# Kernel optimization log

Hardware: AMD Instinct MI355X
Metric: run time of the kernel (lower is better)

## Reference

```python
import jax, jax.numpy as jnp
import numpy as np
import math

B, L, D, H, DFF = 2, 2048, 1024, 16, 4096

def _mha(xq, xkv, Wq, bq, Wk, bk, Wv, bv, Wo, bo, mask, h):
    # xq: [B,Lq,D], xkv: [B,Lk,D], mask: [B,1,Lq,Lk] bool
    b, lq, d = xq.shape
    dk = d // h
    q = (xq @ Wq + bq).reshape(b, lq, h, dk).transpose(0, 2, 1, 3)        # [B,h,Lq,dk]
    k = (xkv @ Wk + bk).reshape(b, -1, h, dk).transpose(0, 2, 1, 3)       # [B,h,Lk,dk]
    v = (xkv @ Wv + bv).reshape(b, -1, h, dk).transpose(0, 2, 1, 3)       # [B,h,Lk,dk]
    scores = jnp.einsum('bhqd,bhkd->bhqk', q, k) / jnp.sqrt(jnp.float32(dk))
    scores = jnp.where(mask, scores, jnp.float32(-1e9))                   # masked_fill(mask==0, -1e9)
    prob = jax.nn.softmax(scores, axis=-1)
    out = jnp.einsum('bhqk,bhkd->bhqd', prob, v)
    out = out.transpose(0, 2, 1, 3).reshape(b, lq, d)
    return out @ Wo + bo

def setup_inputs() -> dict:
    key = jax.random.key(0)
    ks = jax.random.split(key, 16)
    s = 0.02
    inp = {
        'tgt': jax.random.normal(ks[0], (B, L, D), jnp.float32),
        'encoder_out': jax.random.normal(ks[1], (B, L, D), jnp.float32),
        'tgt_mask': jnp.broadcast_to(jnp.tril(jnp.ones((L, L), bool)), (B, 1, L, L)),
        'src_tgt_mask': jnp.ones((B, 1, L, L), bool),
    }
    names = ['sWq','sWk','sWv','sWo','cWq','cWk','cWv','cWo']
    for i, n in enumerate(names):
        inp[n] = s * jax.random.normal(ks[2 + i], (D, D), jnp.float32)
        inp['sb' + n[2] if n[0] == 's' else 'cb' + n[2]] = jnp.zeros((D,), jnp.float32)
    inp['W1'] = s * jax.random.normal(ks[10], (D, DFF), jnp.float32)
    inp['b1'] = jnp.zeros((DFF,), jnp.float32)
    inp['W2'] = s * jax.random.normal(ks[11], (DFF, D), jnp.float32)
    inp['b2'] = jnp.zeros((D,), jnp.float32)
    return inp

def reference(tgt, encoder_out, tgt_mask, src_tgt_mask,
              sWq, sbq, sWk, sbk, sWv, sbv, sWo, sbo,
              cWq, cbq, cWk, cbk, cWv, cbv, cWo, cbo,
              W1, b1, W2, b2):
    # residual 1: masked self-attention (no norm)
    x = tgt + _mha(tgt, tgt, sWq, sbq, sWk, sbk, sWv, sbv, sWo, sbo, tgt_mask, H)
    # residual 2: cross-attention over encoder_out
    x = x + _mha(x, encoder_out, cWq, cbq, cWk, cbk, cWv, cbv, cWo, cbo, src_tgt_mask, H)
    # residual 3: position-wise FFN with ReLU
    x = x + (jax.nn.relu(x @ W1 + b1) @ W2 + b2)
    return x
```

## Files before the change

kernel.cpp:

```cpp
#include <hip/hip_runtime.h>

typedef unsigned short u16;
typedef unsigned int u32;
typedef __attribute__((ext_vector_type(8))) short short8;
typedef __attribute__((ext_vector_type(8))) __bf16 bf16x8;
typedef __attribute__((ext_vector_type(4))) float f32x4;
typedef __attribute__((ext_vector_type(4))) u16 u16x4;
typedef __attribute__((ext_vector_type(2))) u32 u32x2;

#define GLD16(gp, lp) __builtin_amdgcn_global_load_lds( \
    (const __attribute__((address_space(1))) unsigned int*)(gp), \
    (__attribute__((address_space(3))) unsigned int*)(lp), 16, 0, 0)

#if defined(__has_builtin) && __has_builtin(__builtin_amdgcn_exp2f)
#define EXP2(x) __builtin_amdgcn_exp2f(x)
#else
static __device__ __forceinline__ float exp2_asm(float x){
  float r; asm("v_exp_f32 %0, %1" : "=v"(r) : "v"(x)); return r;
}
#define EXP2(x) exp2_asm(x)
#endif

__device__ __forceinline__ float bf2f(u16 u){
  unsigned x = ((unsigned)u) << 16; float f; __builtin_memcpy(&f, &x, 4); return f;
}
__device__ __forceinline__ u16 f2bf(float f){
  unsigned x; __builtin_memcpy(&x, &f, 4);
  x += 0x7fffu + ((x >> 16) & 1u);
  return (u16)(x >> 16);
}
__device__ __forceinline__ u32 pkhi(float lo, float hi){
  u32 a, b; __builtin_memcpy(&a, &lo, 4); __builtin_memcpy(&b, &hi, 4);
  return __builtin_amdgcn_perm(b, a, 0x07060302u);
}
__device__ __forceinline__ f32x4 mfma_bf16(short8 a, short8 b, f32x4 c){
  return __builtin_amdgcn_mfma_f32_16x16x32_bf16(
      __builtin_bit_cast(bf16x8, a), __builtin_bit_cast(bf16x8, b), c, 0, 0, 0);
}

__global__ __launch_bounds__(256) void k_conv(const float* __restrict__ s, u16* __restrict__ d, int n){
  int i4 = (blockIdx.x * 256 + threadIdx.x) * 4;
  if (i4 < n){
    float4 v = *(const float4*)(s + i4);
    u16x4 o; o.x = f2bf(v.x); o.y = f2bf(v.y); o.z = f2bf(v.z); o.w = f2bf(v.w);
    *(u16x4*)(d + i4) = o;
  }
}

__global__ __launch_bounds__(256) void k_transpose(const float* __restrict__ s, u16* __restrict__ d, int K, int N){
  __shared__ float t[32][33];
  int bx = blockIdx.x * 32, by = blockIdx.y * 32;
  int x = threadIdx.x & 31, y = threadIdx.x >> 5;
  #pragma unroll
  for (int i = 0; i < 4; i++)
    t[y + i*8][x] = s[(size_t)(by + y + i*8) * N + bx + x];
  __syncthreads();
  #pragma unroll
  for (int i = 0; i < 4; i++)
    d[(size_t)(bx + y + i*8) * K + by + x] = f2bf(t[x][y + i*8]);
}

struct TP8 { const float* s[8]; u16* d[8]; };
__global__ __launch_bounds__(256) void k_transpose8(TP8 p){
  __shared__ float t[32][33];
  const float* s = p.s[blockIdx.z];
  u16* d = p.d[blockIdx.z];
  int bx = blockIdx.x * 32, by = blockIdx.y * 32;
  int x = threadIdx.x & 31, y = threadIdx.x >> 5;
  #pragma unroll
  for (int i = 0; i < 4; i++)
    t[y + i*8][x] = s[(size_t)(by + y + i*8) * 1024 + bx + x];
  __syncthreads();
  #pragma unroll
  for (int i = 0; i < 4; i++)
    d[(size_t)(bx + y + i*8) * 1024 + by + x] = f2bf(t[x][y + i*8]);
}

__global__ __launch_bounds__(256) void k_packbias(
    const float* __restrict__ sbq, const float* __restrict__ sbk,
    const float* __restrict__ sbv, const float* __restrict__ cbk,
    const float* __restrict__ cbv, float* __restrict__ pbS,
    float* __restrict__ pbC){
  int i = blockIdx.x * 256 + threadIdx.x;
  if (i < 3072) pbS[i] = (i < 1024) ? sbq[i] : (i < 2048 ? sbk[i-1024] : sbv[i-2048]);
  if (i < 2048) pbC[i] = (i < 1024) ? cbk[i] : cbv[i-1024];
}

template<int EPI, int BM, int BN, int KU>
__global__ __launch_bounds__(256, 2) void k_gemm_bt(
    const u16* __restrict__ A, const u16* __restrict__ BT,
    const float* __restrict__ bias, const float* __restrict__ resid,
    float* __restrict__ outF, u16* __restrict__ outB,
    int M, int N, int K, int vt_start, u16* __restrict__ Vt){
  constexpr int MI = BM / 32, NI = BN / 32;
  __shared__ u16 As[2*KU][BM*32];
  __shared__ u16 Bs[2*KU][BN*32];
  int tid = threadIdx.x, wave = tid >> 6, lane = tid & 63;
  int bm = blockIdx.x * BM, bn = blockIdx.y * BN;
  int wm = (wave & 1) * (BM/2), wn = (wave >> 1) * (BN/2);
  int l15 = lane & 15, quad = lane >> 4;

  f32x4 z = {0.f, 0.f, 0.f, 0.f};
  f32x4 acc[MI][NI];
  #pragma unroll
  for (int a = 0; a < MI; a++)
    #pragma unroll
    for (int b = 0; b < NI; b++) acc[a][b] = z;

  int sr = wave*16 + (lane >> 2);
  int sc = ((lane & 3) ^ ((lane >> 3) & 3)) * 8;
  const u16* Ag = A  + (size_t)(bm + sr) * K + sc;
  const u16* Bg = BT + (size_t)(bn + sr) * K + sc;
  int NKP = (K >> 5) / KU;
  int xsw = (l15 >> 1) & 3;

  #pragma unroll
  for (int u = 0; u < KU; u++){
    #pragma unroll
    for (int i = 0; i < BM/64; i++)
      GLD16(Ag + (size_t)(i*64)*K + u*32, &As[u][(wave*16 + i*64) * 32]);
    #pragma unroll
    for (int i = 0; i < BN/64; i++)
      GLD16(Bg + (size_t)(i*64)*K + u*32, &Bs[u][(wave*16 + i*64) * 32]);
  }

  for (int kt = 0; kt < NKP; kt++){
    __syncthreads();
    int cur = (kt & 1) * KU;
    if (kt + 1 < NKP){
      int nb = cur ^ KU;
      #pragma unroll
      for (int u = 0; u < KU; u++){
        int k0 = ((kt + 1) * KU + u) * 32;
        #pragma unroll
        for (int i = 0; i < BM/64; i++)
          GLD16(Ag + (size_t)(i*64)*K + k0, &As[nb+u][(wave*16 + i*64) * 32]);
        #pragma unroll
        for (int i = 0; i < BN/64; i++)
          GLD16(Bg + (size_t)(i*64)*K + k0, &Bs[nb+u][(wave*16 + i*64) * 32]);
      }
    }
    #pragma unroll
    for (int u = 0; u < KU; u++){
      short8 af[MI], bf[NI];
      #pragma unroll
      for (int mi = 0; mi < MI; mi++)
        af[mi] = *(const short8*)&As[cur+u][(wm + mi*16 + l15)*32 + (quad ^ xsw)*8];
      #pragma unroll
      for (int ni = 0; ni < NI; ni++)
        bf[ni] = *(const short8*)&Bs[cur+u][(wn + ni*16 + l15)*32 + (quad ^ xsw)*8];
      #pragma unroll
      for (int mi = 0; mi < MI; mi++)
        #pragma unroll
        for (int ni = 0; ni < NI; ni++)
          acc[mi][ni] = mfma_bf16(af[mi], bf[ni], acc[mi][ni]);
    }
  }

  #pragma unroll
  for (int mi = 0; mi < MI; mi++){
    #pragma unroll
    for (int ni = 0; ni < NI; ni++){
      int col = bn + wn + ni*16 + l15;
      float bv = bias[col];
      if (EPI == 0 && col >= vt_start){
        int vc = col - vt_start;
        int hh = vc >> 6, dd = vc & 63;
        int row0 = bm + wm + mi*16 + quad*4;
        int bb = row0 >> 11, ll = row0 & 2047;
        u16x4 vv;
        #pragma unroll
        for (int r = 0; r < 4; r++) vv[r] = f2bf(acc[mi][ni][r] + bv);
        *(u16x4*)&Vt[(((size_t)bb*16 + hh)*64 + dd)*2048 + ll] = vv;
      } else {
        #pragma unroll
        for (int r = 0; r < 4; r++){
          int row = bm + wm + mi*16 + quad*4 + r;
          float v = acc[mi][ni][r] + bv;
          if (EPI == 1) v = v > 0.f ? v : 0.f;
          size_t idx = (size_t)row * N + col;
          if (EPI >= 2) v += resid[idx];
          if (EPI == 2 || EPI == 3) outF[idx] = v;
          if (EPI != 3) outB[idx] = f2bf(v);
        }
      }
    }
  }
}

template<int EPI>
__global__ __launch_bounds__(256, 4) void k_gemm64(
    const u16* __restrict__ A, const u16* __restrict__ BT,
    const float* __restrict__ bias, const float* __restrict__ resid,
    float* __restrict__ outF, u16* __restrict__ outB,
    int M, int N, int K){
  __shared__ u16 As[4][64*32];
  __shared__ u16 Bs[4][64*32];
  int tid = threadIdx.x, wave = tid >> 6, lane = tid & 63;
  int bm = blockIdx.x * 64, bn = blockIdx.y * 64;
  int wm = (wave & 1) * 32, wn = (wave >> 1) * 32;
  int l15 = lane & 15, quad = lane >> 4;

  f32x4 z = {0.f, 0.f, 0.f, 0.f};
  f32x4 acc[2][2];
  acc[0][0] = z; acc[0][1] = z; acc[1][0] = z; acc[1][1] = z;

  int sr = wave*16 + (lane >> 2);
  int sc = ((lane & 3) ^ ((lane >> 3) & 3)) * 8;
  const u16* Ag = A  + (size_t)(bm + sr) * K + sc;
  const u16* Bg = BT + (size_t)(bn + sr) * K + sc;
  int NT = K >> 5;
  int xsw = (l15 >> 1) & 3;

  #pragma unroll
  for (int s = 0; s < 3; s++){
    GLD16(Ag + s*32, &As[s][(wave*16) * 32]);
    GLD16(Bg + s*32, &Bs[s][(wave*16) * 32]);
  }

  for (int kt = 0; kt < NT; kt++){
    if (kt < NT-2)       asm volatile("s_waitcnt vmcnt(4)" ::: "memory");
    else if (kt == NT-2) asm volatile("s_waitcnt vmcnt(2)" ::: "memory");
    else                 asm volatile("s_waitcnt vmcnt(0)" ::: "memory");
    __builtin_amdgcn_s_barrier();
    if (kt + 3 < NT){
      int s = (kt + 3) & 3, k0 = (kt + 3) * 32;
      GLD16(Ag + k0, &As[s][(wave*16) * 32]);
      GLD16(Bg + k0, &Bs[s][(wave*16) * 32]);
    }
    int cur = kt & 3;
    short8 af[2], bf[2];
    af[0] = *(const short8*)&As[cur][(wm      + l15)*32 + (quad ^ xsw)*8];
    af[1] = *(const short8*)&As[cur][(wm + 16 + l15)*32 + (quad ^ xsw)*8];
    bf[0] = *(const short8*)&Bs[cur][(wn      + l15)*32 + (quad ^ xsw)*8];
    bf[1] = *(const short8*)&Bs[cur][(wn + 16 + l15)*32 + (quad ^ xsw)*8];
    acc[0][0] = mfma_bf16(af[0], bf[0], acc[0][0]);
    acc[0][1] = mfma_bf16(af[0], bf[1], acc[0][1]);
    acc[1][0] = mfma_bf16(af[1], bf[0], acc[1][0]);
    acc[1][1] = mfma_bf16(af[1], bf[1], acc[1][1]);
  }

  #pragma unroll
  for (int mi = 0; mi < 2; mi++){
    #pragma unroll
    for (int ni = 0; ni < 2; ni++){
      int col = bn + wn + ni*16 + l15;
      float bv = bias[col];
      #pragma unroll
      for (int r = 0; r < 4; r++){
        int row = bm + wm + mi*16 + quad*4 + r;
        float v = acc[mi][ni][r] + bv;
        size_t idx = (size_t)row * N + col;
        if (EPI >= 2) v += resid[idx];
        if (EPI == 2 || EPI == 3) outF[idx] = v;
        if (EPI != 3) outB[idx] = f2bf(v);
      }
    }
  }
}

template<bool CAUSAL>
__global__ __launch_bounds__(256, 2) void k_flash(
    const u16* __restrict__ Q, int ldq,
    const u16* __restrict__ Kg, int ldk,
    const u16* __restrict__ Vt,
    u16* __restrict__ O, int ldo){
  __shared__ u16 Ks[2][128*64];
  __shared__ u16 Vs[2][64*128];
  __shared__ u16 Ps[128*64];
  int tid = threadIdx.x, wave = tid >> 6, lane = tid & 63;
  int l15 = lane & 15, quad = lane >> 4;
  int bx = blockIdx.x;
  int qt = CAUSAL ? ((bx & 1) ? (15 - (bx >> 1)) : (bx >> 1)) : bx;
  int bh = blockIdx.y;
  int b = bh >> 4, h = bh & 15;
  size_t bL = (size_t)b * 2048;
  const u16* qp = Q  + (bL + qt*128) * (size_t)ldq + h*64;
  const u16* kp = Kg + bL * (size_t)ldk + h*64;
  const u16* vtp = Vt + (size_t)bh * 64 * 2048;
  int wm = wave * 32;

  const float QSCALE = 0.125f * 1.44269504088896f;
  short8 qf[2][2];
  #pragma unroll
  for (int mi = 0; mi < 2; mi++)
    #pragma unroll
    for (int ks = 0; ks < 2; ks++){
      short8 t = *(const short8*)(qp + (size_t)(wm + mi*16 + l15)*ldq + ks*32 + quad*8);
      #pragma unroll
      for (int j = 0; j < 8; j++)
        t[j] = (short)f2bf(bf2f((u16)t[j]) * QSCALE);
      qf[mi][ks] = t;
    }

  f32x4 z = {0.f, 0.f, 0.f, 0.f};
  f32x4 o[2][4];
  float mrow[2], lrow[2];
  #pragma unroll
  for (int mi = 0; mi < 2; mi++){ mrow[mi] = -3.0e38f; lrow[mi] = 0.f; }
  #pragma unroll
  for (int mi = 0; mi < 2; mi++)
    #pragma unroll
    for (int nd = 0; nd < 4; nd++) o[mi][nd] = z;

  int nkt = CAUSAL ? (qt + 1) : 16;
  int cg = ((lane & 7) ^ ((lane >> 3) & 7)) * 8;
  #pragma unroll
  for (int i = 0; i < 4; i++){
    int r = i*32 + wave*8 + (lane >> 3);
    GLD16(kp + (size_t)r * ldk + cg, &Ks[0][(i*32 + wave*8) * 64]);
  }
  #pragma unroll
  for (int i = 0; i < 4; i++){
    int d0 = i*16 + wave*4;
    int d = d0 + (lane >> 4);
    int j = lane & 15;
    int chunk = (j & 8) | ((j ^ (d & 7)) & 7);
    GLD16(vtp + (size_t)d*2048 + chunk*8, &Vs[0][d0*128]);
  }

  for (int kt = 0; kt < nkt; kt++){
    __syncthreads();
    int cur = kt & 1;
    if (kt + 1 < nkt){
      int nb = cur ^ 1;
      #pragma unroll
      for (int i = 0; i < 4; i++){
        int r = i*32 + wave*8 + (lane >> 3);
        GLD16(kp + (size_t)((kt+1)*128 + r) * ldk + cg, &Ks[nb][(i*32 + wave*8) * 64]);
      }
      #pragma unroll
      for (int i = 0; i < 4; i++){
        int d0 = i*16 + wave*4;
        int d = d0 + (lane >> 4);
        int j = lane & 15;
        int chunk = (j & 8) | ((j ^ (d & 7)) & 7);
        GLD16(vtp + (size_t)d*2048 + (kt+1)*128 + chunk*8, &Vs[nb][d0*128]);
      }
    }

    f32x4 s[2][8];
    #pragma unroll
    for (int mi = 0; mi < 2; mi++)
      #pragma unroll
      for (int nk = 0; nk < 8; nk++) s[mi][nk] = z;
    #pragma unroll
    for (int ks = 0; ks < 2; ks++){
      short8 kf[8];
      #pragma unroll
      for (int nk = 0; nk < 8; nk++){
        int row = nk*16 + l15;
        kf[nk] = *(const short8*)&Ks[cur][row*64 + (((ks*4 + quad) ^ (row & 7)))*8];
      }
      #pragma unroll
      for (int mi = 0; mi < 2; mi++)
        #pragma unroll
        for (int nk = 0; nk < 8; nk++)
          s[mi][nk] = mfma_bf16(kf[nk], qf[mi][ks], s[mi][nk]);
    }

    if (CAUSAL && kt == qt){
      #pragma unroll
      for (int mi = 0; mi < 2; mi++){
        int q = wm + mi*16 + l15;
        #pragma unroll
        for (int nk = 0; nk < 8; nk++)
          #pragma unroll
          for (int r = 0; r < 4; r++){
            int key = nk*16 + quad*4 + r;
            if (key > q) s[mi][nk][r] = -1e30f;
          }
      }
    }

    #pragma unroll
    for (int mi = 0; mi < 2; mi++){
      float mx = s[mi][0][0];
      #pragma unroll
      for (int nk = 0; nk < 8; nk++)
        #pragma unroll
        for (int r = 0; r < 4; r++) mx = fmaxf(mx, s[mi][nk][r]);
      mx = fmaxf(mx, __shfl_xor(mx, 16));
      mx = fmaxf(mx, __shfl_xor(mx, 32));
      if (!__all(mx - mrow[mi] <= 8.f)){
        float mnew = fmaxf(mrow[mi], mx);
        float alpha = EXP2(mrow[mi] - mnew);
        mrow[mi] = mnew;
        lrow[mi] *= alpha;
        #pragma unroll
        for (int r = 0; r < 4; r++){
          float ar = __shfl(alpha, quad*20 + r);
          #pragma unroll
          for (int nd = 0; nd < 4; nd++) o[mi][nd][r] *= ar;
        }
      }
      float ls = 0.f;
      #pragma unroll
      for (int nk = 0; nk < 8; nk++)
        #pragma unroll
        for (int r = 0; r < 4; r++){
          float p = EXP2(s[mi][nk][r] - mrow[mi]);
          s[mi][nk][r] = p;
          ls += p;
        }
      ls += __shfl_xor(ls, 16);
      ls += __shfl_xor(ls, 32);
      lrow[mi] += ls;
    }

    #pragma unroll
    for (int half = 0; half < 2; half++){
      #pragma unroll
      for (int mi = 0; mi < 2; mi++){
        int row = wm + mi*16 + l15;
        #pragma unroll
        for (int nkl = 0; nkl < 4; nkl++){
          int nk = half*4 + nkl;
          u32x2 pw;
          pw.x = pkhi(s[mi][nk][0], s[mi][nk][1]);
          pw.y = pkhi(s[mi][nk][2], s[mi][nk][3]);
          int c = nkl*4 + quad;
          int phys = c ^ (row & 14);
          *(u32x2*)&Ps[row*64 + phys*4] = pw;
        }
      }
      #pragma unroll
      for (int kcl = 0; kcl < 2; kcl++){
        int kc = half*2 + kcl;
        short8 vf[4], pf[2];
        #pragma unroll
        for (int nd = 0; nd < 4; nd++){
          int d = nd*16 + l15;
          int cc = kc*4 + quad;
          int phys = (cc & 8) | ((cc ^ (d & 7)) & 7);
          vf[nd] = *(const short8*)&Vs[cur][d*128 + phys*8];
        }
        #pragma unroll
        for (int mi = 0; mi < 2; mi++){
          int row = wm + mi*16 + l15;
          int pc = kcl*8 + quad*2;
          int pphys = pc ^ (row & 14);
          pf[mi] = *(const short8*)&Ps[row*64 + pphys*4];
        }
        #pragma unroll
        for (int mi = 0; mi < 2; mi++)
          #pragma unroll
          for (int nd = 0; nd < 4; nd++)
            o[mi][nd] = mfma_bf16(pf[mi], vf[nd], o[mi][nd]);
      }
    }
  }

  u16* op = O + (bL + qt*128) * (size_t)ldo + h*64;
  #pragma unroll
  for (int mi = 0; mi < 2; mi++){
    float invl = 1.f / lrow[mi];
    #pragma unroll
    for (int r = 0; r < 4; r++){
      float ir = __shfl(invl, quad*20 + r);
      #pragma unroll
      for (int nd = 0; nd < 4; nd++)
        op[(size_t)(wm + mi*16 + quad*4 + r)*ldo + nd*16 + l15] = f2bf(o[mi][nd][r] * ir);
    }
  }
}

extern "C" void kernel_launch(void* const* d_in, const int* in_sizes, int n_in,
                              void* d_out, int out_size, void* d_ws, size_t ws_size,
                              hipStream_t stream){
  (void)in_sizes; (void)n_in; (void)out_size; (void)ws_size;
  const float* tgt = (const float*)d_in[0];
  const float* enc = (const float*)d_in[1];
  const float* sWq = (const float*)d_in[4];  const float* sbq = (const float*)d_in[5];
  const float* sWk = (const float*)d_in[6];  const float* sbk = (const float*)d_in[7];
  const float* sWv = (const float*)d_in[8];  const float* sbv = (const float*)d_in[9];
  const float* sWo = (const float*)d_in[10]; const float* sbo = (const float*)d_in[11];
  const float* cWq = (const float*)d_in[12]; const float* cbq = (const float*)d_in[13];
  const float* cWk = (const float*)d_in[14]; const float* cbk = (const float*)d_in[15];
  const float* cWv = (const float*)d_in[16]; const float* cbv = (const float*)d_in[17];
  const float* cWo = (const float*)d_in[18]; const float* cbo = (const float*)d_in[19];
  const float* W1  = (const float*)d_in[20]; const float* b1  = (const float*)d_in[21];
  const float* W2  = (const float*)d_in[22]; const float* b2  = (const float*)d_in[23];
  float* out = (float*)d_out;

  const int M = 4096;
  const int NEVER = 1 << 30;
  char* w = (char*)d_ws;
  auto alloc = [&](size_t bytes)->void*{ void* p = w; w += (bytes + 255) & ~(size_t)255; return p; };
  u16* tb    = (u16*)alloc((size_t)M*1024*2);
  u16* eb    = (u16*)alloc((size_t)M*1024*2);
  u16* qkv   = (u16*)alloc((size_t)M*3072*2);
  u16* ao    = (u16*)alloc((size_t)M*1024*2);
  u16* xb    = (u16*)alloc((size_t)M*1024*2);
  float* x1f = (float*)alloc((size_t)M*1024*4);
  u16* hbuf  = (u16*)alloc((size_t)M*4096*2);
  u16* VtS   = (u16*)alloc((size_t)32*64*2048*2);
  u16* VtC   = (u16*)alloc((size_t)32*64*2048*2);
  u16* sQKVT = (u16*)alloc((size_t)3072*1024*2);
  u16* sWoT  = (u16*)alloc((size_t)1024*1024*2);
  u16* cWqT  = (u16*)alloc((size_t)1024*1024*2);
  u16* cKVT  = (u16*)alloc((size_t)2048*1024*2);
  u16* cWoT  = (u16*)alloc((size_t)1024*1024*2);
  u16* W1T   = (u16*)alloc((size_t)4096*1024*2);
  u16* W2T   = (u16*)alloc((size_t)1024*4096*2);
  float* pbS = (float*)alloc(3072*4);
  float* pbC = (float*)alloc(2048*4);
  u16* cq  = tb;
  u16* ckv = qkv;

  k_conv<<<dim3(4096), 256, 0, stream>>>(tgt, tb, M*1024);
  k_conv<<<dim3(4096), 256, 0, stream>>>(enc, eb, M*1024);
  TP8 tp;
  tp.s[0]=sWq; tp.s[1]=sWk; tp.s[2]=sWv; tp.s[3]=sWo;
  tp.s[4]=cWq; tp.s[5]=cWk; tp.s[6]=cWv; tp.s[7]=cWo;
  tp.d[0]=sQKVT; tp.d[1]=sQKVT+1024*1024; tp.d[2]=sQKVT+2048*1024; tp.d[3]=sWoT;
  tp.d[4]=cWqT; tp.d[5]=cKVT; tp.d[6]=cKVT+1024*1024; tp.d[7]=cWoT;
  k_transpose8<<<dim3(32,32,8), 256, 0, stream>>>(tp);
  k_transpose<<<dim3(128,32), 256, 0, stream>>>(W1, W1T, 1024, 4096);
  k_transpose<<<dim3(32,128), 256, 0, stream>>>(W2, W2T, 4096, 1024);
  k_packbias<<<dim3(12), 256, 0, stream>>>(sbq, sbk, sbv, cbk, cbv, pbS, pbC);

  k_gemm_bt<0,128,128,1><<<dim3(32,24), 256, 0, stream>>>(tb, sQKVT, pbS, nullptr, nullptr, qkv, M, 3072, 1024, 2048, VtS);
  k_flash<true><<<dim3(16,32), 256, 0, stream>>>(qkv, 3072, qkv+1024, 3072, VtS, ao, 1024);
  k_gemm64<2><<<dim3(64,16), 256, 0, stream>>>(ao, sWoT, sbo, tgt, x1f, xb, M, 1024, 1024);

  k_gemm64<0><<<dim3(64,16), 256, 0, stream>>>(xb, cWqT, cbq, nullptr, nullptr, cq, M, 1024, 1024);
  k_gemm_bt<0,128,128,1><<<dim3(32,16), 256, 0, stream>>>(eb, cKVT, pbC, nullptr, nullptr, ckv, M, 2048, 1024, 1024, VtC);
  k_flash<false><<<dim3(16,32), 256, 0, stream>>>(cq, 1024, ckv, 2048, VtC, ao, 1024);
  k_gemm64<2><<<dim3(64,16), 256, 0, stream>>>(ao, cWoT, cbo, x1f, x1f, xb, M, 1024, 1024);

  k_gemm_bt<1,128,128,1><<<dim3(32,32), 256, 0, stream>>>(xb, W1T, b1, nullptr, nullptr, hbuf, M, 4096, 1024, NEVER, nullptr);
  k_gemm64<3><<<dim3(64,16), 256, 0, stream>>>(hbuf, W2T, b2, x1f, out, nullptr, M, 1024, 4096);
}
```

Baseline: 545.4 us.

## Double k-step per barrier in 64x64 GEMM and XCD-swizzle flash attention blocks

The 64x64 GEMM now processes two 32-wide k-slices per barrier from a 6-slot LDS ring, prefetching two slices ahead. This halves the barrier and waitcnt overhead per unit of work. The cost is larger shared memory and occupancy lowered from 4 to 2 blocks. Separately, flash attention remaps block indices so that consecutive workgroups on the same XCD handle neighbouring heads and tiles, which is meant to improve L2 locality.

After: 569.5 us. 1.04x slower.

```diff
diff --git a/kernel.cpp b/kernel.cpp
--- a/kernel.cpp
+++ b/kernel.cpp
@@ -36,6 +36,14 @@
 __device__ __forceinline__ f32x4 mfma_bf16(short8 a, short8 b, f32x4 c){
   return __builtin_amdgcn_mfma_f32_16x16x32_bf16(
       __builtin_bit_cast(bf16x8, a), __builtin_bit_cast(bf16x8, b), c, 0, 0, 0);
+}
+
+__device__ __forceinline__ void xcd_swz(int& bx, int& by){
+  int gx = gridDim.x;
+  int nwg = gx * gridDim.y;
+  int l = by * gx + bx;
+  int s = (l & 7) * (nwg >> 3) + (l >> 3);
+  bx = s % gx; by = s / gx;
 }
 
 __global__ __launch_bounds__(256) void k_conv(const float* __restrict__ s, u16* __restrict__ d, int n){
@@ -189,13 +197,13 @@
 }
 
 template<int EPI>
-__global__ __launch_bounds__(256, 4) void k_gemm64(
+__global__ __launch_bounds__(256, 2) void k_gemm64r3(
     const u16* __restrict__ A, const u16* __restrict__ BT,
     const float* __restrict__ bias, const float* __restrict__ resid,
     float* __restrict__ outF, u16* __restrict__ outB,
     int M, int N, int K){
-  __shared__ u16 As[4][64*32];
-  __shared__ u16 Bs[4][64*32];
+  __shared__ u16 As[6][64*32];
+  __shared__ u16 Bs[6][64*32];
   int tid = threadIdx.x, wave = tid >> 6, lane = tid & 63;
   int bm = blockIdx.x * 64, bn = blockIdx.y * 64;
   int wm = (wave & 1) * 32, wn = (wave >> 1) * 32;
@@ -209,35 +217,43 @@
   int sc = ((lane & 3) ^ ((lane >> 3) & 3)) * 8;
   const u16* Ag = A  + (size_t)(bm + sr) * K + sc;
   const u16* Bg = BT + (size_t)(bn + sr) * K + sc;
-  int NT = K >> 5;
+  int NG = K >> 6;
   int xsw = (l15 >> 1) & 3;
 
   #pragma unroll
-  for (int s = 0; s < 3; s++){
-    GLD16(Ag + s*32, &As[s][(wave*16) * 32]);
-    GLD16(Bg + s*32, &Bs[s][(wave*16) * 32]);
-  }
-
-  for (int kt = 0; kt < NT; kt++){
-    if (kt < NT-2)       asm volatile("s_waitcnt vmcnt(4)" ::: "memory");
-    else if (kt == NT-2) asm volatile("s_waitcnt vmcnt(2)" ::: "memory");
-    else                 asm volatile("s_waitcnt vmcnt(0)" ::: "memory");
+  for (int g = 0; g < 2; g++)
+    #pragma unroll
+    for (int u = 0; u < 2; u++){
+      GLD16(Ag + (g*2+u)*32, &As[g*2+u][(wave*16) * 32]);
+      GLD16(Bg + (g*2+u)*32, &Bs[g*2+u][(wave*16) * 32]);
+    }
+
+  int cslot = 0, pslot = 4;
+  for (int g = 0; g < NG; g++){
+    if (g + 1 < NG) asm volatile("s_waitcnt vmcnt(4)" ::: "memory");
+    else            asm volatile("s_waitcnt vmcnt(0)" ::: "memory");
     __builtin_amdgcn_s_barrier();
-    if (kt + 3 < NT){
-      int s = (kt + 3) & 3, k0 = (kt + 3) * 32;
-      GLD16(Ag + k0, &As[s][(wave*16) * 32]);
-      GLD16(Bg + k0, &Bs[s][(wave*16) * 32]);
-    }
-    int cur = kt & 3;
-    short8 af[2], bf[2];
-    af[0] = *(const short8*)&As[cur][(wm      + l15)*32 + (quad ^ xsw)*8];
-    af[1] = *(const short8*)&As[cur][(wm + 16 + l15)*32 + (quad ^ xsw)*8];
-    bf[0] = *(const short8*)&Bs[cur][(wn      + l15)*32 + (quad ^ xsw)*8];
-    bf[1] = *(const short8*)&Bs[cur][(wn + 16 + l15)*32 + (quad ^ xsw)*8];
-    acc[0][0] = mfma_bf16(af[0], bf[0], acc[0][0]);
-    acc[0][1] = mfma_bf16(af[0], bf[1], acc[0][1]);
-    acc[1][0] = mfma_bf16(af[1], bf[0], acc[1][0]);
-    acc[1][1] = mfma_bf16(af[1], bf[1], acc[1][1]);
+    if (g + 2 < NG){
+      int k0 = (g + 2) * 64;
+      GLD16(Ag + k0,      &As[pslot  ][(wave*16) * 32]);
+      GLD16(Bg + k0,      &Bs[pslot  ][(wave*16) * 32]);
+      GLD16(Ag + k0 + 32, &As[pslot+1][(wave*16) * 32]);
+      GLD16(Bg + k0 + 32, &Bs[pslot+1][(wave*16) * 32]);
+    }
+    #pragma unroll
+    for (int u = 0; u < 2; u++){
+      short8 af[2], bf[2];
+      af[0] = *(const short8*)&As[cslot+u][(wm      + l15)*32 + (quad ^ xsw)*8];
+      af[1] = *(const short8*)&As[cslot+u][(wm + 16 + l15)*32 + (quad ^ xsw)*8];
+      bf[0] = *(const short8*)&Bs[cslot+u][(wn      + l15)*32 + (quad ^ xsw)*8];
+      bf[1] = *(const short8*)&Bs[cslot+u][(wn + 16 + l15)*32 + (quad ^ xsw)*8];
+      acc[0][0] = mfma_bf16(af[0], bf[0], acc[0][0]);
+      acc[0][1] = mfma_bf16(af[0], bf[1], acc[0][1]);
+      acc[1][0] = mfma_bf16(af[1], bf[0], acc[1][0]);
+      acc[1][1] = mfma_bf16(af[1], bf[1], acc[1][1]);
+    }
+    cslot += 2; if (cslot == 6) cslot = 0;
+    pslot += 2; if (pslot == 6) pslot = 0;
   }
 
   #pragma unroll
@@ -270,9 +286,9 @@
   __shared__ u16 Ps[128*64];
   int tid = threadIdx.x, wave = tid >> 6, lane = tid & 63;
   int l15 = lane & 15, quad = lane >> 4;
-  int bx = blockIdx.x;
+  int bx = blockIdx.x, bh = blockIdx.y;
+  xcd_swz(bx, bh);
   int qt = CAUSAL ? ((bx & 1) ? (15 - (bx >> 1)) : (bx >> 1)) : bx;
-  int bh = blockIdx.y;
   int b = bh >> 4, h = bh & 15;
   size_t bL = (size_t)b * 2048;
   const u16* qp = Q  + (bL + qt*128) * (size_t)ldq + h*64;
@@ -522,13 +538,13 @@
 
   k_gemm_bt<0,128,128,1><<<dim3(32,24), 256, 0, stream>>>(tb, sQKVT, pbS, nullptr, nullptr, qkv, M, 3072, 1024, 2048, VtS);
   k_flash<true><<<dim3(16,32), 256, 0, stream>>>(qkv, 3072, qkv+1024, 3072, VtS, ao, 1024);
-  k_gemm64<2><<<dim3(64,16), 256, 0, stream>>>(ao, sWoT, sbo, tgt, x1f, xb, M, 1024, 1024);
-
-  k_gemm64<0><<<dim3(64,16), 256, 0, stream>>>(xb, cWqT, cbq, nullptr, nullptr, cq, M, 1024, 1024);
+  k_gemm64r3<2><<<dim3(64,16), 256, 0, stream>>>(ao, sWoT, sbo, tgt, x1f, xb, M, 1024, 1024);
+
+  k_gemm64r3<0><<<dim3(64,16), 256, 0, stream>>>(xb, cWqT, cbq, nullptr, nullptr, cq, M, 1024, 1024);
   k_gemm_bt<0,128,128,1><<<dim3(32,16), 256, 0, stream>>>(eb, cKVT, pbC, nullptr, nullptr, ckv, M, 2048, 1024, 1024, VtC);
   k_flash<false><<<dim3(16,32), 256, 0, stream>>>(cq, 1024, ckv, 2048, VtC, ao, 1024);
-  k_gemm64<2><<<dim3(64,16), 256, 0, stream>>>(ao, cWoT, cbo, x1f, x1f, xb, M, 1024, 1024);
+  k_gemm64r3<2><<<dim3(64,16), 256, 0, stream>>>(ao, cWoT, cbo, x1f, x1f, xb, M, 1024, 1024);
 
   k_gemm_bt<1,128,128,1><<<dim3(32,32), 256, 0, stream>>>(xb, W1T, b1, nullptr, nullptr, hbuf, M, 4096, 1024, NEVER, nullptr);
-  k_gemm64<3><<<dim3(64,16), 256, 0, stream>>>(hbuf, W2T, b2, x1f, out, nullptr, M, 1024, 4096);
-}
+  k_gemm64r3<3><<<dim3(64,16), 256, 0, stream>>>(hbuf, W2T, b2, x1f, out, nullptr, M, 1024, 4096);
+}
```
